# Kernel optimization log

Measured on AMD Instinct MI355X. Metric: run time of the kernel, lower is better.

## Reference

```python
import jax, jax.numpy as jnp
import numpy as np

DIM = 96
HEADS = 8  # num_heads_v
EPS = 1e-12  # torch F.normalize eps


def conv1x1(x, w, b):
    # x: [B,C,H,W], w: [O,C,1,1], b: [O]
    y = jnp.einsum('bchw,oc->bohw', x, w[:, :, 0, 0])
    return y + b[None, :, None, None]


def dwconv3x3(x, w, b):
    # depthwise 3x3, groups == channels; w: [C,1,3,3]
    y = jax.lax.conv_general_dilated(
        x, w, window_strides=(1, 1), padding=((1, 1), (1, 1)),
        dimension_numbers=('NCHW', 'OIHW', 'NCHW'),
        feature_group_count=x.shape[1])
    return y + b[None, :, None, None]


def setup_inputs() -> dict:
    key = jax.random.key(0)
    ks = jax.random.split(key, 7)
    c = DIM
    s = 0.05
    x = jax.random.normal(ks[0], (4, c, 256, 256), jnp.float32)
    qkv_w = jax.random.normal(ks[1], (3 * c, c, 1, 1), jnp.float32) * s
    qkv_b = jax.random.normal(ks[2], (3 * c,), jnp.float32) * s
    dw_w = jax.random.normal(ks[3], (3 * c, 1, 3, 3), jnp.float32) * s
    dw_b = jax.random.normal(ks[4], (3 * c,), jnp.float32) * s
    proj_w = jax.random.normal(ks[5], (c, c, 1, 1), jnp.float32) * s
    proj_b = jax.random.normal(ks[6], (c,), jnp.float32) * s
    temperature = jnp.ones((HEADS, 1, 1), jnp.float32)
    return {"x": x, "qkv_w": qkv_w, "qkv_b": qkv_b, "dw_w": dw_w,
            "dw_b": dw_b, "proj_w": proj_w, "proj_b": proj_b,
            "temperature": temperature}


def reference(x, qkv_w, qkv_b, dw_w, dw_b, proj_w, proj_b, temperature):
    b, c, h, w = x.shape
    head = temperature.shape[0]
    w2 = w // head
    qkv = dwconv3x3(conv1x1(x, qkv_w, qkv_b), dw_w, dw_b)
    q0, k0, v0 = jnp.split(qkv, 3, axis=1)  # each [b,c,h,w]

    def to_heads(t):
        # 'b c h (head w2) -> b head w2 (c h)'
        t = t.reshape(b, c, h, head, w2)
        return jnp.transpose(t, (0, 3, 4, 1, 2)).reshape(b, head, w2, c * h)

    q = to_heads(q0)
    k = to_heads(k0)
    v = to_heads(v0)
    q = q / jnp.maximum(jnp.linalg.norm(q, axis=-1, keepdims=True), EPS)
    k = k / jnp.maximum(jnp.linalg.norm(k, axis=-1, keepdims=True), EPS)
    attn = jnp.einsum('bhid,bhjd->bhij', q, k) * temperature[None]  # [b,head,w2,w2]
    attn = jax.nn.softmax(attn, axis=-1)
    out = jnp.einsum('bhij,bhjd->bhid', attn, v)  # [b,head,w2,c*h]
    # 'b head w2 (c h) -> b c h (head w2)'
    out = out.reshape(b, head, w2, c, h)
    out = jnp.transpose(out, (0, 3, 4, 1, 2)).reshape(b, c, h, w)
    return conv1x1(out, proj_w, proj_b)
```

## Files before the change

### kernel.cpp

```cpp
#include <hip/hip_runtime.h>

#define CC 96
#define C3 288
#define HH 256
#define WW 256
#define HWC 65536
#define NHEADS 8
#define W2 32

typedef __bf16 bf16x8 __attribute__((ext_vector_type(8)));
typedef float f32x4 __attribute__((ext_vector_type(4)));
typedef unsigned short us8v __attribute__((ext_vector_type(8)));

__device__ __forceinline__ float bf2f(unsigned short u) {
  return __uint_as_float(((unsigned)u) << 16);
}
__device__ __forceinline__ unsigned short f2bf(float f) {
  unsigned u = __float_as_uint(f);
  unsigned r = u + 0x7fffu + ((u >> 16) & 1u);
  return (unsigned short)(r >> 16);
}

__global__ __launch_bounds__(256, 4) void k1_qkv_mfma(
    const float* __restrict__ x, const float* __restrict__ qw,
    const float* __restrict__ qb, unsigned short* __restrict__ pre, int b0)
{
  __shared__ __align__(16) unsigned short As2[2][64 * 106];
  const int t = threadIdx.x;
  const int o0 = blockIdx.y * 96;
  const int bz = blockIdx.z;
  const float* xb = x + (size_t)(b0 + bz) * CC * HWC;

  const int wave = t >> 6, lane = t & 63;
  const int wm = wave & 1, wn = wave >> 1;
  const int row = lane & 15, kg = lane >> 4;

  bf16x8 bfr[3][3];
  float bias[3];
#pragma unroll
  for (int nt = 0; nt < 3; ++nt) {
    int ocl = wn * 48 + nt * 16 + row;
    bias[nt] = qb[o0 + ocl];
#pragma unroll
    for (int kk = 0; kk < 3; ++kk) {
      const float* wp = qw + (size_t)(o0 + ocl) * 96 + kk * 32 + kg * 8;
      float4 w0 = *reinterpret_cast<const float4*>(wp);
      float4 w1 = *reinterpret_cast<const float4*>(wp + 4);
      us8v u;
      u[0] = f2bf(w0.x); u[1] = f2bf(w0.y); u[2] = f2bf(w0.z); u[3] = f2bf(w0.w);
      u[4] = f2bf(w1.x); u[5] = f2bf(w1.y); u[6] = f2bf(w1.z); u[7] = f2bf(w1.w);
      bfr[kk][nt] = *reinterpret_cast<bf16x8*>(&u);
    }
  }

  int sic[3], sp4[3];
#pragma unroll
  for (int r = 0; r < 3; ++r) {
    int lin = r * 256 + t;
    sic[r] = lin >> 4;
    sp4[r] = (lin & 15) * 4;
  }

  int p0 = blockIdx.x * 512;
  float4 va0[3], va1[3];
#pragma unroll
  for (int r = 0; r < 3; ++r) {
    va0[r] = *reinterpret_cast<const float4*>(xb + (size_t)(2 * sic[r]) * HWC + p0 + sp4[r]);
    va1[r] = *reinterpret_cast<const float4*>(xb + (size_t)(2 * sic[r] + 1) * HWC + p0 + sp4[r]);
  }

  for (int i = 0; i < 8; ++i) {
    unsigned short* Ac = As2[i & 1];
#pragma unroll
    for (int r = 0; r < 3; ++r) {
      float a0[4] = {va0[r].x, va0[r].y, va0[r].z, va0[r].w};
      float a1[4] = {va1[r].x, va1[r].y, va1[r].z, va1[r].w};
#pragma unroll
      for (int j = 0; j < 4; ++j) {
        unsigned pk = (unsigned)f2bf(a0[j]) | ((unsigned)f2bf(a1[j]) << 16);
        *reinterpret_cast<unsigned*>(&Ac[(sp4[r] + j) * 106 + 2 * sic[r]]) = pk;
      }
    }
    if (i < 7) {
      int p0n = p0 + 64;
#pragma unroll
      for (int r = 0; r < 3; ++r) {
        va0[r] = *reinterpret_cast<const float4*>(xb + (size_t)(2 * sic[r]) * HWC + p0n + sp4[r]);
        va1[r] = *reinterpret_cast<const float4*>(xb + (size_t)(2 * sic[r] + 1) * HWC + p0n + sp4[r]);
      }
    }
    __syncthreads();

    f32x4 acc[2][3];
#pragma unroll
    for (int mt = 0; mt < 2; ++mt)
#pragma unroll
      for (int nt = 0; nt < 3; ++nt) acc[mt][nt] = (f32x4){0.f, 0.f, 0.f, 0.f};
#pragma unroll
    for (int kk = 0; kk < 3; ++kk) {
      bf16x8 a[2];
#pragma unroll
      for (int mt = 0; mt < 2; ++mt)
        a[mt] = *reinterpret_cast<const bf16x8*>(
            &Ac[(wm * 32 + mt * 16 + row) * 106 + kk * 32 + kg * 8]);
#pragma unroll
      for (int mt = 0; mt < 2; ++mt)
#pragma unroll
        for (int nt = 0; nt < 3; ++nt)
          acc[mt][nt] = __builtin_amdgcn_mfma_f32_16x16x32_bf16(
              a[mt], bfr[kk][nt], acc[mt][nt], 0, 0, 0);
    }
    __syncthreads();

    unsigned short* tD = (unsigned short*)As2;
#pragma unroll
    for (int nt = 0; nt < 3; ++nt) {
      int ocl = wn * 48 + nt * 16 + row;
      float bv = bias[nt];
#pragma unroll
      for (int mt = 0; mt < 2; ++mt) {
        int pxl = wm * 32 + mt * 16 + kg * 4;
        f32x4 v = acc[mt][nt];
        unsigned pk0 = (unsigned)f2bf(v[0] + bv) | ((unsigned)f2bf(v[1] + bv) << 16);
        unsigned pk1 = (unsigned)f2bf(v[2] + bv) | ((unsigned)f2bf(v[3] + bv) << 16);
        *reinterpret_cast<unsigned*>(&tD[ocl * 72 + pxl]) = pk0;
        *reinterpret_cast<unsigned*>(&tD[ocl * 72 + pxl + 2]) = pk1;
      }
    }
    __syncthreads();
    unsigned short* preb = pre + ((size_t)bz * C3 + o0) * HWC + p0;
#pragma unroll
    for (int r = 0; r < 3; ++r) {
      int lin = r * 256 + t;
      int oc = lin >> 3, ch = lin & 7;
      us8v v = *reinterpret_cast<const us8v*>(&tD[oc * 72 + ch * 8]);
      *reinterpret_cast<us8v*>(preb + (size_t)oc * HWC + ch * 8) = v;
    }
    __syncthreads();
    p0 += 64;
  }
}

__global__ __launch_bounds__(256) void k2_dw(
    const unsigned short* __restrict__ pre, const float* __restrict__ dww,
    const float* __restrict__ dwb, unsigned short* __restrict__ dwo)
{
  const int t = threadIdx.x;
  const int c3 = blockIdx.x;
  const int hb = blockIdx.y;
  const int bz = blockIdx.z;
  const size_t choff_in  = ((size_t)bz * C3 + c3) * HWC;
  const size_t choff_out = ((size_t)bz * 192 + c3) * HWC;
  const int team = t >> 5, tl = t & 31;
  const int h0 = hb * 32 + team * 4;

  us8v rin[6];
#pragma unroll
  for (int r = 0; r < 6; ++r) {
    int hh = h0 - 1 + r;
    if (hh >= 0 && hh < HH)
      rin[r] = *reinterpret_cast<const us8v*>(pre + choff_in + (size_t)hh * WW + tl * 8);
    else
      rin[r] = (us8v){0, 0, 0, 0, 0, 0, 0, 0};
  }

  float wg[9];
#pragma unroll
  for (int i = 0; i < 9; ++i) wg[i] = dww[c3 * 9 + i];
  const float bias = dwb[c3];

  float f[6][8];
  float lf[6], rt[6];
#pragma unroll
  for (int r = 0; r < 6; ++r) {
#pragma unroll
    for (int j = 0; j < 8; ++j) f[r][j] = bf2f(rin[r][j]);
    float l = __shfl_up(f[r][7], 1, 32);
    float rr = __shfl_down(f[r][0], 1, 32);
    lf[r] = (tl == 0) ? 0.f : l;
    rt[r] = (tl == 31) ? 0.f : rr;
  }

#pragma unroll
  for (int orow = 0; orow < 4; ++orow) {
    float o[8];
#pragma unroll
    for (int j = 0; j < 8; ++j) o[j] = bias;
#pragma unroll
    for (int k = 0; k < 3; ++k) {
      const int r = orow + k;
      const float w0 = wg[k * 3 + 0], w1 = wg[k * 3 + 1], w2 = wg[k * 3 + 2];
      o[0] = fmaf(lf[r], w0, fmaf(f[r][0], w1, fmaf(f[r][1], w2, o[0])));
#pragma unroll
      for (int j = 1; j < 7; ++j)
        o[j] = fmaf(f[r][j - 1], w0, fmaf(f[r][j], w1, fmaf(f[r][j + 1], w2, o[j])));
      o[7] = fmaf(f[r][6], w0, fmaf(f[r][7], w1, fmaf(rt[r], w2, o[7])));
    }
    us8v u;
#pragma unroll
    for (int j = 0; j < 8; ++j) u[j] = f2bf(o[j]);
    *reinterpret_cast<us8v*>((unsigned short*)dwo + choff_out + (size_t)(h0 + orow) * WW + tl * 8) = u;
  }
}

__global__ __launch_bounds__(256, 4) void k3_gram(
    const unsigned short* __restrict__ dwo, float* __restrict__ gpart,
    float* __restrict__ ssq)
{
  __shared__ __align__(16) unsigned short qT[32 * 264];
  __shared__ __align__(16) unsigned short kT[32 * 264];
  const int t = threadIdx.x;
  const int cg0 = blockIdx.x;
  const int head = blockIdx.y, bz = blockIdx.z;
  const int lane = t & 63, wave = t >> 6;
  const int mt = wave & 1, nt = wave >> 1;
  const int l15 = lane & 15, l4 = lane >> 4;
  const int cg = t & 7;
  int rp[4];
#pragma unroll
  for (int r = 0; r < 4; ++r) rp[r] = (r * 256 + t) >> 3;

  const unsigned short* qbase = dwo + ((size_t)bz * 192 + cg0 * 4) * HWC + head * W2;
  const unsigned short* kbase = qbase + (size_t)CC * HWC;

  ushort4 qa[4], qb_[4], ka[4], kb_[4];
#pragma unroll
  for (int r = 0; r < 4; ++r) {
    qa[r] = *reinterpret_cast<const ushort4*>(qbase + (size_t)(2 * rp[r]) * WW + cg * 4);
    qb_[r] = *reinterpret_cast<const ushort4*>(qbase + (size_t)(2 * rp[r] + 1) * WW + cg * 4);
    ka[r] = *reinterpret_cast<const ushort4*>(kbase + (size_t)(2 * rp[r]) * WW + cg * 4);
    kb_[r] = *reinterpret_cast<const ushort4*>(kbase + (size_t)(2 * rp[r] + 1) * WW + cg * 4);
  }

  f32x4 acc = (f32x4){0.f, 0.f, 0.f, 0.f};
  float ssum_q = 0.f, ssum_k = 0.f;

  for (int cc = 0; cc < 4; ++cc) {
#pragma unroll
    for (int r = 0; r < 4; ++r) {
      unsigned short aq0[4] = {qa[r].x, qa[r].y, qa[r].z, qa[r].w};
      unsigned short aq1[4] = {qb_[r].x, qb_[r].y, qb_[r].z, qb_[r].w};
      unsigned short ak0[4] = {ka[r].x, ka[r].y, ka[r].z, ka[r].w};
      unsigned short ak1[4] = {kb_[r].x, kb_[r].y, kb_[r].z, kb_[r].w};
#pragma unroll
      for (int j = 0; j < 4; ++j) {
        int dwi = (cg * 4 + j) * 132 + rp[r];
        *(reinterpret_cast<unsigned*>(qT) + dwi) =
            (unsigned)aq0[j] | ((unsigned)aq1[j] << 16);
        *(reinterpret_cast<unsigned*>(kT) + dwi) =
            (unsigned)ak0[j] | ((unsigned)ak1[j] << 16);
      }
    }
    if (cc < 3) {
      const unsigned short* qn = qbase + (size_t)(cc + 1) * HWC;
      const unsigned short* kn = kbase + (size_t)(cc + 1) * HWC;
#pragma unroll
      for (int r = 0; r < 4; ++r) {
        qa[r] = *reinterpret_cast<const ushort4*>(qn + (size_t)(2 * rp[r]) * WW + cg * 4);
        qb_[r] = *reinterpret_cast<const ushort4*>(qn + (size_t)(2 * rp[r] + 1) * WW + cg * 4);
        ka[r] = *reinterpret_cast<const ushort4*>(kn + (size_t)(2 * rp[r]) * WW + cg * 4);
        kb_[r] = *reinterpret_cast<const ushort4*>(kn + (size_t)(2 * rp[r] + 1) * WW + cg * 4);
      }
    }
    __builtin_amdgcn_sched_barrier(0);
    __syncthreads();
#pragma unroll
    for (int kk = 0; kk < 8; ++kk) {
      bf16x8 a = *reinterpret_cast<const bf16x8*>(
          &qT[(mt * 16 + l15) * 264 + kk * 32 + l4 * 8]);
      bf16x8 b = *reinterpret_cast<const bf16x8*>(
          &kT[(nt * 16 + l15) * 264 + kk * 32 + l4 * 8]);
      acc = __builtin_amdgcn_mfma_f32_16x16x32_bf16(a, b, acc, 0, 0, 0);
    }
    {
      const int i = t & 31, seg = t >> 5;
#pragma unroll
      for (int m = 0; m < 4; ++m) {
        us8v vq = *reinterpret_cast<const us8v*>(&qT[i * 264 + seg * 32 + m * 8]);
        us8v vk = *reinterpret_cast<const us8v*>(&kT[i * 264 + seg * 32 + m * 8]);
#pragma unroll
        for (int e = 0; e < 8; ++e) {
          float fq = bf2f(vq[e]), fk = bf2f(vk[e]);
          ssum_q = fmaf(fq, fq, ssum_q);
          ssum_k = fmaf(fk, fk, ssum_k);
        }
      }
    }
    __syncthreads();
  }

  float* gp = gpart + (((size_t)bz * NHEADS + head) * 24 + cg0) * 1024;
#pragma unroll
  for (int reg = 0; reg < 4; ++reg)
    gp[(nt * 16 + l15) * 32 + mt * 16 + l4 * 4 + reg] = acc[reg];

  float* red = reinterpret_cast<float*>(qT);
  red[t] = ssum_q;
  red[256 + t] = ssum_k;
  __syncthreads();
  if (t < 32) {
    float sq = 0.f, sk = 0.f;
#pragma unroll
    for (int p = 0; p < 8; ++p) { sq += red[t + 32 * p]; sk += red[256 + t + 32 * p]; }
    atomicAdd(&ssq[(size_t)bz * 512 + head * W2 + t], sq);
    atomicAdd(&ssq[(size_t)bz * 512 + 256 + head * W2 + t], sk);
  }
}

__global__ __launch_bounds__(256) void k4b_softmax(
    const float* __restrict__ gpart, const float* __restrict__ ssq,
    const float* __restrict__ temp, float* __restrict__ attn)
{
  __shared__ float lg[1024];
  const int t = threadIdx.x;
  const int head = blockIdx.x, bz = blockIdx.y;
  const float* gp = gpart + ((size_t)bz * NHEADS + head) * 24 * 1024;
  float4 s = make_float4(0.f, 0.f, 0.f, 0.f);
#pragma unroll 4
  for (int cg = 0; cg < 24; ++cg) {
    float4 v = *reinterpret_cast<const float4*>(gp + cg * 1024 + t * 4);
    s.x += v.x; s.y += v.y; s.z += v.z; s.w += v.w;
  }
  *reinterpret_cast<float4*>(&lg[t * 4]) = s;
  __syncthreads();
  if (t < 32) {
    const int i = t;
    const float* sq_ = ssq + (size_t)bz * 512 + head * W2;
    const float* sk_ = ssq + (size_t)bz * 512 + 256 + head * W2;
    float invq = 1.f / fmaxf(sqrtf(sq_[i]), 1e-12f);
    float tpq = temp[head] * invq;
    float rowv[32];
    float m = -1e30f;
#pragma unroll
    for (int j = 0; j < 32; ++j) {
      float invk = 1.f / fmaxf(sqrtf(sk_[j]), 1e-12f);
      float v = lg[j * 32 + i] * tpq * invk;
      rowv[j] = v;
      m = fmaxf(m, v);
    }
    float ssum = 0;
#pragma unroll
    for (int j = 0; j < 32; ++j) { rowv[j] = expf(rowv[j] - m); ssum += rowv[j]; }
    float inv = 1.f / ssum;
    float* ap = attn + ((size_t)bz * NHEADS + head) * 1024 + i * 32;
#pragma unroll
    for (int j = 0; j < 32; ++j) ap[j] = rowv[j] * inv;
  }
}

__global__ __launch_bounds__(256) void k5a_attnv(
    const unsigned short* __restrict__ pre, const float* __restrict__ dww,
    const float* __restrict__ dwb, const float* __restrict__ attn,
    unsigned short* __restrict__ tbuf)
{
  __shared__ __align__(16) unsigned short vsm[64 * 264];
  __shared__ __align__(16) unsigned short atn_s[256 * 36];
  const int t = threadIdx.x;
  const int tile = blockIdx.x;
  const int bz = blockIdx.y;
  const size_t R0 = (size_t)tile * 64;
  const int c = tile >> 2;
  const int h0 = (tile & 3) * 64;
  const unsigned short* vsrc = pre + ((size_t)bz * C3 + 2 * CC + c) * HWC;
  const int team = t >> 5, tl = t & 31;

  float4 av[8];
  {
    const float* ap = attn + (size_t)bz * 8192 + t * 32;
#pragma unroll
    for (int k = 0; k < 8; ++k)
      av[k] = *reinterpret_cast<const float4*>(ap + k * 4);
  }

  float wg[9];
#pragma unroll
  for (int i = 0; i < 9; ++i) wg[i] = dww[(2 * CC + c) * 9 + i];
  const float vbias = dwb[2 * CC + c];

#pragma unroll
  for (int p = 0; p < 2; ++p) {
    const int hb = h0 + team * 8 + p * 4;
    us8v rin[6];
#pragma unroll
    for (int r = 0; r < 6; ++r) {
      int hh = hb - 1 + r;
      if (hh >= 0 && hh < HH)
        rin[r] = *reinterpret_cast<const us8v*>(vsrc + (size_t)hh * WW + tl * 8);
      else
        rin[r] = (us8v){0, 0, 0, 0, 0, 0, 0, 0};
    }
    float f[6][8], lf[6], rt[6];
#pragma unroll
    for (int r = 0; r < 6; ++r) {
#pragma unroll
      for (int j = 0; j < 8; ++j) f[r][j] = bf2f(rin[r][j]);
      float l = __shfl_up(f[r][7], 1, 32);
      float rr = __shfl_down(f[r][0], 1, 32);
      lf[r] = (tl == 0) ? 0.f : l;
      rt[r] = (tl == 31) ? 0.f : rr;
    }
#pragma unroll
    for (int orow = 0; orow < 4; ++orow) {
      float o[8];
#pragma unroll
      for (int j = 0; j < 8; ++j) o[j] = vbias;
#pragma unroll
      for (int k = 0; k < 3; ++k) {
        const int r = orow + k;
        const float w0 = wg[k * 3 + 0], w1 = wg[k * 3 + 1], w2 = wg[k * 3 + 2];
        o[0] = fmaf(lf[r], w0, fmaf(f[r][0], w1, fmaf(f[r][1], w2, o[0])));
#pragma unroll
        for (int j = 1; j < 7; ++j)
          o[j] = fmaf(f[r][j - 1], w0, fmaf(f[r][j], w1, fmaf(f[r][j + 1], w2, o[j])));
        o[7] = fmaf(f[r][6], w0, fmaf(f[r][7], w1, fmaf(rt[r], w2, o[7])));
      }
      us8v u;
#pragma unroll
      for (int j = 0; j < 8; ++j) u[j] = f2bf(o[j]);
      int rl = team * 8 + p * 4 + orow;
      *reinterpret_cast<us8v*>(&vsm[rl * 264 + tl * 8]) = u;
    }
  }
#pragma unroll
  for (int k = 0; k < 8; ++k) {
    ushort4 u;
    u.x = f2bf(av[k].x); u.y = f2bf(av[k].y); u.z = f2bf(av[k].z); u.w = f2bf(av[k].w);
    *reinterpret_cast<ushort4*>(&atn_s[t * 36 + k * 4]) = u;
  }
  __syncthreads();

  const int wave = t >> 6, lane = t & 63;
  const int mrow = lane & 15, kg = lane >> 4;

  bf16x8 a[8], b[16];
#pragma unroll
  for (int hd = 0; hd < 8; ++hd)
    a[hd] = *reinterpret_cast<const bf16x8*>(
        &vsm[(wave * 16 + mrow) * 264 + hd * 32 + kg * 8]);
#pragma unroll
  for (int hd = 0; hd < 8; ++hd)
#pragma unroll
    for (int it = 0; it < 2; ++it)
      b[hd * 2 + it] = *reinterpret_cast<const bf16x8*>(
          &atn_s[(hd * 32 + it * 16 + mrow) * 36 + kg * 8]);

  f32x4 acc[16];
#pragma unroll
  for (int q = 0; q < 16; ++q) acc[q] = (f32x4){0.f, 0.f, 0.f, 0.f};
#pragma unroll
  for (int hd = 0; hd < 8; ++hd)
#pragma unroll
    for (int it = 0; it < 2; ++it)
      acc[hd * 2 + it] = __builtin_amdgcn_mfma_f32_16x16x32_bf16(
          a[hd], b[hd * 2 + it], acc[hd * 2 + it], 0, 0, 0);
  __syncthreads();

#pragma unroll
  for (int hd = 0; hd < 8; ++hd)
#pragma unroll
    for (int it = 0; it < 2; ++it) {
      f32x4 v = acc[hd * 2 + it];
      int col = hd * 32 + it * 16 + mrow;
#pragma unroll
      for (int r = 0; r < 4; ++r)
        vsm[(wave * 16 + kg * 4 + r) * 264 + col] = f2bf(v[r]);
    }
  unsigned short* tdst = tbuf + (size_t)bz * CC * HWC + R0 * 256;
#pragma unroll
  for (int k = 0; k < 8; ++k) {
    int n = k * 64 + lane;
    int rloc = n >> 5, c8 = n & 31;
    us8v v = *reinterpret_cast<const us8v*>(&vsm[(wave * 16 + rloc) * 264 + c8 * 8]);
    *reinterpret_cast<us8v*>(tdst + ((size_t)(wave * 16 + rloc)) * 256 + c8 * 8) = v;
  }
}

__global__ __launch_bounds__(256, 4) void k5b_proj(
    const unsigned short* __restrict__ tbuf, const float* __restrict__ pw,
    const float* __restrict__ pb, float* __restrict__ out, int b0)
{
  __shared__ __align__(16) unsigned short As2[2][64 * 106];
  const int t = threadIdx.x;
  const int bz = blockIdx.y;
  const unsigned short* tb = tbuf + (size_t)bz * CC * HWC;

  const int wave = t >> 6, lane = t & 63;
  const int wm = wave & 1, wn = wave >> 1;
  const int row = lane & 15, kg = lane >> 4;

  bf16x8 bfr[3][3];
  float bias[3];
#pragma unroll
  for (int nt = 0; nt < 3; ++nt) {
    int ocl = wn * 48 + nt * 16 + row;
    bias[nt] = pb[ocl];
#pragma unroll
    for (int kk = 0; kk < 3; ++kk) {
      const float* wp = pw + (size_t)ocl * 96 + kk * 32 + kg * 8;
      float4 w0 = *reinterpret_cast<const float4*>(wp);
      float4 w1 = *reinterpret_cast<const float4*>(wp + 4);
      us8v u;
      u[0] = f2bf(w0.x); u[1] = f2bf(w0.y); u[2] = f2bf(w0.z); u[3] = f2bf(w0.w);
      u[4] = f2bf(w1.x); u[5] = f2bf(w1.y); u[6] = f2bf(w1.z); u[7] = f2bf(w1.w);
      bfr[kk][nt] = *reinterpret_cast<bf16x8*>(&u);
    }
  }

  int sic[3], sp4[3];
#pragma unroll
  for (int r = 0; r < 3; ++r) {
    int lin = r * 256 + t;
    sic[r] = lin >> 4;
    sp4[r] = (lin & 15) * 4;
  }

  int p0 = blockIdx.x * 512;
  ushort4 ua0[3], ua1[3];
#pragma unroll
  for (int r = 0; r < 3; ++r) {
    ua0[r] = *reinterpret_cast<const ushort4*>(tb + (size_t)(2 * sic[r]) * HWC + p0 + sp4[r]);
    ua1[r] = *reinterpret_cast<const ushort4*>(tb + (size_t)(2 * sic[r] + 1) * HWC + p0 + sp4[r]);
  }

  for (int i = 0; i < 8; ++i) {
    unsigned short* Ac = As2[i & 1];
#pragma unroll
    for (int r = 0; r < 3; ++r) {
      unsigned short a0[4] = {ua0[r].x, ua0[r].y, ua0[r].z, ua0[r].w};
      unsigned short a1[4] = {ua1[r].x, ua1[r].y, ua1[r].z, ua1[r].w};
#pragma unroll
      for (int j = 0; j < 4; ++j) {
        unsigned pk = (unsigned)a0[j] | ((unsigned)a1[j] << 16);
        *reinterpret_cast<unsigned*>(&Ac[(sp4[r] + j) * 106 + 2 * sic[r]]) = pk;
      }
    }
    if (i < 7) {
      int p0n = p0 + 64;
#pragma unroll
      for (int r = 0; r < 3; ++r) {
        ua0[r] = *reinterpret_cast<const ushort4*>(tb + (size_t)(2 * sic[r]) * HWC + p0n + sp4[r]);
        ua1[r] = *reinterpret_cast<const ushort4*>(tb + (size_t)(2 * sic[r] + 1) * HWC + p0n + sp4[r]);
      }
    }
    __syncthreads();

    f32x4 acc[2][3];
#pragma unroll
    for (int mt = 0; mt < 2; ++mt)
#pragma unroll
      for (int nt = 0; nt < 3; ++nt) acc[mt][nt] = (f32x4){0.f, 0.f, 0.f, 0.f};
#pragma unroll
    for (int kk = 0; kk < 3; ++kk) {
      bf16x8 a[2];
#pragma unroll
      for (int mt = 0; mt < 2; ++mt)
        a[mt] = *reinterpret_cast<const bf16x8*>(
            &Ac[(wm * 32 + mt * 16 + row) * 106 + kk * 32 + kg * 8]);
#pragma unroll
      for (int mt = 0; mt < 2; ++mt)
#pragma unroll
        for (int nt = 0; nt < 3; ++nt)
          acc[mt][nt] = __builtin_amdgcn_mfma_f32_16x16x32_bf16(
              a[mt], bfr[kk][nt], acc[mt][nt], 0, 0, 0);
    }
    __syncthreads();

    float* tD = (float*)As2;
#pragma unroll
    for (int nt = 0; nt < 3; ++nt) {
      int ocl = wn * 48 + nt * 16 + row;
      float bv = bias[nt];
#pragma unroll
      for (int mt = 0; mt < 2; ++mt) {
        int pxl = wm * 32 + mt * 16 + kg * 4;
        f32x4 v = acc[mt][nt];
        float4 w = make_float4(v[0] + bv, v[1] + bv, v[2] + bv, v[3] + bv);
        *reinterpret_cast<float4*>(&tD[ocl * 68 + pxl]) = w;
      }
    }
    __syncthreads();
    float* ob = out + (size_t)(b0 + bz) * CC * HWC + p0;
#pragma unroll
    for (int r = 0; r < 6; ++r) {
      int lin = r * 256 + t;
      int o = lin >> 4, p4 = (lin & 15) * 4;
      float4 v = *reinterpret_cast<const float4*>(&tD[o * 68 + p4]);
      *reinterpret_cast<float4*>(ob + (size_t)o * HWC + p4) = v;
    }
    __syncthreads();
    p0 += 64;
  }
}

extern "C" void kernel_launch(void* const* d_in, const int* in_sizes, int n_in,
                              void* d_out, int out_size, void* d_ws, size_t ws_size,
                              hipStream_t stream)
{
  const float* x      = (const float*)d_in[0];
  const float* qkv_w  = (const float*)d_in[1];
  const float* qkv_b  = (const float*)d_in[2];
  const float* dw_w   = (const float*)d_in[3];
  const float* dw_b   = (const float*)d_in[4];
  const float* proj_w = (const float*)d_in[5];
  const float* proj_b = (const float*)d_in[6];
  const float* temp   = (const float*)d_in[7];
  float* out = (float*)d_out;

  const size_t per_pre   = (size_t)C3 * HWC * 2;
  const size_t per_dwo   = (size_t)192 * HWC * 2;
  const size_t per_tbuf  = (size_t)CC * HWC * 2;
  const size_t per_ssq   = (size_t)2 * 256 * 4;
  const size_t per_attn  = (size_t)NHEADS * 1024 * 4;
  const size_t per_gpart = (size_t)NHEADS * 24 * 1024 * 4;
  const size_t per_b = per_pre + per_dwo + per_tbuf + per_ssq + per_attn + per_gpart;

  int bc = 4;
  while (bc > 1 && per_b * (size_t)bc > ws_size) bc >>= 1;

  char* p = (char*)d_ws;
  unsigned short* pre  = (unsigned short*)p; p += per_pre * bc;
  unsigned short* dwo  = (unsigned short*)p; p += per_dwo * bc;
  unsigned short* tbuf = (unsigned short*)p; p += per_tbuf * bc;
  float* ssq   = (float*)p; p += per_ssq * bc;
  float* attn  = (float*)p; p += per_attn * bc;
  float* gpart = (float*)p; p += per_gpart * bc;

  for (int b0 = 0; b0 < 4; b0 += bc) {
    k1_qkv_mfma<<<dim3(128, 3, bc), 256, 0, stream>>>(x, qkv_w, qkv_b, pre, b0);
    k2_dw<<<dim3(192, 8, bc), 256, 0, stream>>>(pre, dw_w, dw_b, dwo);
    hipMemsetAsync(ssq, 0, per_ssq * bc, stream);
    k3_gram<<<dim3(24, NHEADS, bc), 256, 0, stream>>>(dwo, gpart, ssq);
    k4b_softmax<<<dim3(NHEADS, bc), 256, 0, stream>>>(gpart, ssq, temp, attn);
    k5a_attnv<<<dim3(384, bc), 256, 0, stream>>>(pre, dw_w, dw_b, attn, tbuf);
    k5b_proj<<<dim3(128, bc), 256, 0, stream>>>(tbuf, proj_w, proj_b, out, b0);
  }
}
```

Before: 223.2 us.

## Fuse depthwise 3x3 conv for q/k into the Gram kernel, drop dwo buffer

The separate depthwise-conv kernel that wrote q and k to an intermediate bf16 buffer is removed. The Gram kernel now reads the pre-conv tensor, computes the 3x3 depthwise conv for its head slice in registers, and writes the result straight into shared memory for the MFMA. Squared norms are taken from the fp32 conv outputs rather than re-read from shared memory. This drops a full write and read of the q/k intermediate. The cost is extra compute and halo loads inside the Gram kernel, plus one extra barrier before reuse of shared memory.

Measured after the change: 222.9 us, median of 2. Within noise of the previous version (-0.1%).

```diff
diff --git a/kernel.cpp b/kernel.cpp
--- a/kernel.cpp
+++ b/kernel.cpp
@@ -141,70 +141,9 @@
   }
 }
 
-__global__ __launch_bounds__(256) void k2_dw(
+__global__ __launch_bounds__(256, 4) void k3_gram(
     const unsigned short* __restrict__ pre, const float* __restrict__ dww,
-    const float* __restrict__ dwb, unsigned short* __restrict__ dwo)
-{
-  const int t = threadIdx.x;
-  const int c3 = blockIdx.x;
-  const int hb = blockIdx.y;
-  const int bz = blockIdx.z;
-  const size_t choff_in  = ((size_t)bz * C3 + c3) * HWC;
-  const size_t choff_out = ((size_t)bz * 192 + c3) * HWC;
-  const int team = t >> 5, tl = t & 31;
-  const int h0 = hb * 32 + team * 4;
-
-  us8v rin[6];
-#pragma unroll
-  for (int r = 0; r < 6; ++r) {
-    int hh = h0 - 1 + r;
-    if (hh >= 0 && hh < HH)
-      rin[r] = *reinterpret_cast<const us8v*>(pre + choff_in + (size_t)hh * WW + tl * 8);
-    else
-      rin[r] = (us8v){0, 0, 0, 0, 0, 0, 0, 0};
-  }
-
-  float wg[9];
-#pragma unroll
-  for (int i = 0; i < 9; ++i) wg[i] = dww[c3 * 9 + i];
-  const float bias = dwb[c3];
-
-  float f[6][8];
-  float lf[6], rt[6];
-#pragma unroll
-  for (int r = 0; r < 6; ++r) {
-#pragma unroll
-    for (int j = 0; j < 8; ++j) f[r][j] = bf2f(rin[r][j]);
-    float l = __shfl_up(f[r][7], 1, 32);
-    float rr = __shfl_down(f[r][0], 1, 32);
-    lf[r] = (tl == 0) ? 0.f : l;
-    rt[r] = (tl == 31) ? 0.f : rr;
-  }
-
-#pragma unroll
-  for (int orow = 0; orow < 4; ++orow) {
-    float o[8];
-#pragma unroll
-    for (int j = 0; j < 8; ++j) o[j] = bias;
-#pragma unroll
-    for (int k = 0; k < 3; ++k) {
-      const int r = orow + k;
-      const float w0 = wg[k * 3 + 0], w1 = wg[k * 3 + 1], w2 = wg[k * 3 + 2];
-      o[0] = fmaf(lf[r], w0, fmaf(f[r][0], w1, fmaf(f[r][1], w2, o[0])));
-#pragma unroll
-      for (int j = 1; j < 7; ++j)
-        o[j] = fmaf(f[r][j - 1], w0, fmaf(f[r][j], w1, fmaf(f[r][j + 1], w2, o[j])));
-      o[7] = fmaf(f[r][6], w0, fmaf(f[r][7], w1, fmaf(rt[r], w2, o[7])));
-    }
-    us8v u;
-#pragma unroll
-    for (int j = 0; j < 8; ++j) u[j] = f2bf(o[j]);
-    *reinterpret_cast<us8v*>((unsigned short*)dwo + choff_out + (size_t)(h0 + orow) * WW + tl * 8) = u;
-  }
-}
-
-__global__ __launch_bounds__(256, 4) void k3_gram(
-    const unsigned short* __restrict__ dwo, float* __restrict__ gpart,
+    const float* __restrict__ dwb, float* __restrict__ gpart,
     float* __restrict__ ssq)
 {
   __shared__ __align__(16) unsigned short qT[32 * 264];
@@ -215,54 +154,101 @@
   const int lane = t & 63, wave = t >> 6;
   const int mt = wave & 1, nt = wave >> 1;
   const int l15 = lane & 15, l4 = lane >> 4;
-  const int cg = t & 7;
-  int rp[4];
-#pragma unroll
-  for (int r = 0; r < 4; ++r) rp[r] = (r * 256 + t) >> 3;
-
-  const unsigned short* qbase = dwo + ((size_t)bz * 192 + cg0 * 4) * HWC + head * W2;
-  const unsigned short* kbase = qbase + (size_t)CC * HWC;
-
-  ushort4 qa[4], qb_[4], ka[4], kb_[4];
-#pragma unroll
-  for (int r = 0; r < 4; ++r) {
-    qa[r] = *reinterpret_cast<const ushort4*>(qbase + (size_t)(2 * rp[r]) * WW + cg * 4);
-    qb_[r] = *reinterpret_cast<const ushort4*>(qbase + (size_t)(2 * rp[r] + 1) * WW + cg * 4);
-    ka[r] = *reinterpret_cast<const ushort4*>(kbase + (size_t)(2 * rp[r]) * WW + cg * 4);
-    kb_[r] = *reinterpret_cast<const ushort4*>(kbase + (size_t)(2 * rp[r] + 1) * WW + cg * 4);
-  }
+  const int hgroup = t >> 2;
+  const int lw = t & 3;
+  const int h0 = hgroup * 4;
+  const int w0 = head * W2 + lw * 8;
 
   f32x4 acc = (f32x4){0.f, 0.f, 0.f, 0.f};
   float ssum_q = 0.f, ssum_k = 0.f;
+  float o[4][8];
 
   for (int cc = 0; cc < 4; ++cc) {
-#pragma unroll
-    for (int r = 0; r < 4; ++r) {
-      unsigned short aq0[4] = {qa[r].x, qa[r].y, qa[r].z, qa[r].w};
-      unsigned short aq1[4] = {qb_[r].x, qb_[r].y, qb_[r].z, qb_[r].w};
-      unsigned short ak0[4] = {ka[r].x, ka[r].y, ka[r].z, ka[r].w};
-      unsigned short ak1[4] = {kb_[r].x, kb_[r].y, kb_[r].z, kb_[r].w};
-#pragma unroll
-      for (int j = 0; j < 4; ++j) {
-        int dwi = (cg * 4 + j) * 132 + rp[r];
-        *(reinterpret_cast<unsigned*>(qT) + dwi) =
-            (unsigned)aq0[j] | ((unsigned)aq1[j] << 16);
-        *(reinterpret_cast<unsigned*>(kT) + dwi) =
-            (unsigned)ak0[j] | ((unsigned)ak1[j] << 16);
-      }
-    }
-    if (cc < 3) {
-      const unsigned short* qn = qbase + (size_t)(cc + 1) * HWC;
-      const unsigned short* kn = kbase + (size_t)(cc + 1) * HWC;
-#pragma unroll
-      for (int r = 0; r < 4; ++r) {
-        qa[r] = *reinterpret_cast<const ushort4*>(qn + (size_t)(2 * rp[r]) * WW + cg * 4);
-        qb_[r] = *reinterpret_cast<const ushort4*>(qn + (size_t)(2 * rp[r] + 1) * WW + cg * 4);
-        ka[r] = *reinterpret_cast<const ushort4*>(kn + (size_t)(2 * rp[r]) * WW + cg * 4);
-        kb_[r] = *reinterpret_cast<const ushort4*>(kn + (size_t)(2 * rp[r] + 1) * WW + cg * 4);
-      }
-    }
-    __builtin_amdgcn_sched_barrier(0);
+    const int cq = cg0 * 4 + cc;
+#pragma unroll
+    for (int tensor = 0; tensor < 2; ++tensor) {
+      const int ch = (tensor ? CC : 0) + cq;
+      const unsigned short* src = pre + ((size_t)bz * C3 + ch) * HWC;
+      const float* wg9 = dww + ch * 9;
+      const float bias = dwb[ch];
+
+      us8v rin[6];
+#pragma unroll
+      for (int r = 0; r < 6; ++r) {
+        int hh = h0 - 1 + r;
+        rin[r] = (hh >= 0 && hh < HH)
+            ? *reinterpret_cast<const us8v*>(src + (size_t)hh * WW + w0)
+            : (us8v){0, 0, 0, 0, 0, 0, 0, 0};
+      }
+      float eL[6], eR[6];
+#pragma unroll
+      for (int r = 0; r < 6; ++r) { eL[r] = 0.f; eR[r] = 0.f; }
+      if (lw == 0 && head > 0) {
+#pragma unroll
+        for (int r = 0; r < 6; ++r) {
+          int hh = h0 - 1 + r;
+          if (hh >= 0 && hh < HH) eL[r] = bf2f(src[(size_t)hh * WW + w0 - 1]);
+        }
+      }
+      if (lw == 3 && head < 7) {
+#pragma unroll
+        for (int r = 0; r < 6; ++r) {
+          int hh = h0 - 1 + r;
+          if (hh >= 0 && hh < HH) eR[r] = bf2f(src[(size_t)hh * WW + w0 + 8]);
+        }
+      }
+      float f[6][8], lf[6], rt[6];
+#pragma unroll
+      for (int r = 0; r < 6; ++r) {
+#pragma unroll
+        for (int j = 0; j < 8; ++j) f[r][j] = bf2f(rin[r][j]);
+        float l = __shfl_up(f[r][7], 1);
+        float rr = __shfl_down(f[r][0], 1);
+        lf[r] = (lw == 0) ? eL[r] : l;
+        rt[r] = (lw == 3) ? eR[r] : rr;
+      }
+#pragma unroll
+      for (int orow = 0; orow < 4; ++orow) {
+#pragma unroll
+        for (int j = 0; j < 8; ++j) o[orow][j] = bias;
+#pragma unroll
+        for (int k = 0; k < 3; ++k) {
+          const int r = orow + k;
+          const float w0_ = wg9[k * 3 + 0], w1_ = wg9[k * 3 + 1], w2_ = wg9[k * 3 + 2];
+          o[orow][0] = fmaf(lf[r], w0_, fmaf(f[r][0], w1_, fmaf(f[r][1], w2_, o[orow][0])));
+#pragma unroll
+          for (int j = 1; j < 7; ++j)
+            o[orow][j] = fmaf(f[r][j - 1], w0_, fmaf(f[r][j], w1_, fmaf(f[r][j + 1], w2_, o[orow][j])));
+          o[orow][7] = fmaf(f[r][6], w0_, fmaf(f[r][7], w1_, fmaf(rt[r], w2_, o[orow][7])));
+        }
+      }
+      if (tensor == 0) {
+        __syncthreads();
+        unsigned* dst = reinterpret_cast<unsigned*>(qT);
+#pragma unroll
+        for (int j = 0; j < 8; ++j)
+#pragma unroll
+          for (int p = 0; p < 2; ++p)
+            dst[(lw * 8 + j) * 132 + hgroup * 2 + p] =
+                (unsigned)f2bf(o[2 * p][j]) | ((unsigned)f2bf(o[2 * p + 1][j]) << 16);
+#pragma unroll
+        for (int orow = 0; orow < 4; ++orow)
+#pragma unroll
+          for (int j = 0; j < 8; ++j) ssum_q = fmaf(o[orow][j], o[orow][j], ssum_q);
+      } else {
+        unsigned* dst = reinterpret_cast<unsigned*>(kT);
+#pragma unroll
+        for (int j = 0; j < 8; ++j)
+#pragma unroll
+          for (int p = 0; p < 2; ++p)
+            dst[(lw * 8 + j) * 132 + hgroup * 2 + p] =
+                (unsigned)f2bf(o[2 * p][j]) | ((unsigned)f2bf(o[2 * p + 1][j]) << 16);
+#pragma unroll
+        for (int orow = 0; orow < 4; ++orow)
+#pragma unroll
+          for (int j = 0; j < 8; ++j) ssum_k = fmaf(o[orow][j], o[orow][j], ssum_k);
+      }
+    }
     __syncthreads();
 #pragma unroll
     for (int kk = 0; kk < 8; ++kk) {
@@ -272,21 +258,6 @@
           &kT[(nt * 16 + l15) * 264 + kk * 32 + l4 * 8]);
       acc = __builtin_amdgcn_mfma_f32_16x16x32_bf16(a, b, acc, 0, 0, 0);
     }
-    {
-      const int i = t & 31, seg = t >> 5;
-#pragma unroll
-      for (int m = 0; m < 4; ++m) {
-        us8v vq = *reinterpret_cast<const us8v*>(&qT[i * 264 + seg * 32 + m * 8]);
-        us8v vk = *reinterpret_cast<const us8v*>(&kT[i * 264 + seg * 32 + m * 8]);
-#pragma unroll
-        for (int e = 0; e < 8; ++e) {
-          float fq = bf2f(vq[e]), fk = bf2f(vk[e]);
-          ssum_q = fmaf(fq, fq, ssum_q);
-          ssum_k = fmaf(fk, fk, ssum_k);
-        }
-      }
-    }
-    __syncthreads();
   }
 
   float* gp = gpart + (((size_t)bz * NHEADS + head) * 24 + cg0) * 1024;
@@ -294,6 +265,7 @@
   for (int reg = 0; reg < 4; ++reg)
     gp[(nt * 16 + l15) * 32 + mt * 16 + l4 * 4 + reg] = acc[reg];
 
+  __syncthreads();
   float* red = reinterpret_cast<float*>(qT);
   red[t] = ssum_q;
   red[256 + t] = ssum_k;
@@ -607,19 +579,17 @@
   float* out = (float*)d_out;
 
   const size_t per_pre   = (size_t)C3 * HWC * 2;
-  const size_t per_dwo   = (size_t)192 * HWC * 2;
   const size_t per_tbuf  = (size_t)CC * HWC * 2;
   const size_t per_ssq   = (size_t)2 * 256 * 4;
   const size_t per_attn  = (size_t)NHEADS * 1024 * 4;
   const size_t per_gpart = (size_t)NHEADS * 24 * 1024 * 4;
-  const size_t per_b = per_pre + per_dwo + per_tbuf + per_ssq + per_attn + per_gpart;
+  const size_t per_b = per_pre + per_tbuf + per_ssq + per_attn + per_gpart;
 
   int bc = 4;
   while (bc > 1 && per_b * (size_t)bc > ws_size) bc >>= 1;
 
   char* p = (char*)d_ws;
   unsigned short* pre  = (unsigned short*)p; p += per_pre * bc;
-  unsigned short* dwo  = (unsigned short*)p; p += per_dwo * bc;
   unsigned short* tbuf = (unsigned short*)p; p += per_tbuf * bc;
   float* ssq   = (float*)p; p += per_ssq * bc;
   float* attn  = (float*)p; p += per_attn * bc;
@@ -627,9 +597,8 @@
 
   for (int b0 = 0; b0 < 4; b0 += bc) {
     k1_qkv_mfma<<<dim3(128, 3, bc), 256, 0, stream>>>(x, qkv_w, qkv_b, pre, b0);
-    k2_dw<<<dim3(192, 8, bc), 256, 0, stream>>>(pre, dw_w, dw_b, dwo);
     hipMemsetAsync(ssq, 0, per_ssq * bc, stream);
-    k3_gram<<<dim3(24, NHEADS, bc), 256, 0, stream>>>(dwo, gpart, ssq);
+    k3_gram<<<dim3(24, NHEADS, bc), 256, 0, stream>>>(pre, dw_w, dw_b, gpart, ssq);
     k4b_softmax<<<dim3(NHEADS, bc), 256, 0, stream>>>(gpart, ssq, temp, attn);
     k5a_attnv<<<dim3(384, bc), 256, 0, stream>>>(pre, dw_w, dw_b, attn, tbuf);
     k5b_proj<<<dim3(128, bc), 256, 0, stream>>>(tbuf, proj_w, proj_b, out, b0);
```
